# Optimization experiments

Hardware: AMD Instinct MI355X
Metric: run time of the kernel (lower is better)

## Reference

```python
import jax, jax.numpy as jnp
import numpy as np

N, INC, INN, OUTC, OUTN, MAXD = 8, 64, 20000, 64, 8000, 32


def setup_inputs() -> dict:
    key = jax.random.key(0)
    k0, k1, k2, k3, k4 = jax.random.split(key, 5)
    # adjacency list: outn nodes, degree in [8, 32], padded to MAXD with index 0
    rng = np.random.default_rng(0)
    deg = rng.integers(8, MAXD + 1, size=OUTN)                      # (outn,)
    A_np = rng.integers(0, INN, size=(OUTN, MAXD))                  # (outn, maxD)
    valid = np.arange(MAXD)[None, :] < deg[:, None]
    A_np = np.where(valid, A_np, 0)
    # '_norm' option: mask entries are 1/degree for valid slots, 0 for pad
    mask_np = valid.astype(np.float32) / deg[:, None].astype(np.float32)

    x = jax.random.normal(k0, (N, INC, INN), dtype=jnp.float32)
    # hadamard weight: sqrt(2/inn) * U(-1, 1)
    weight = np.sqrt(2.0 / INN).astype(np.float32) * (
        2.0 * jax.random.uniform(k1, (INC, INN), dtype=jnp.float32) - 1.0)
    # weight_norm Linear(inc, outc): v (outc, inc) direction, g (outc,) magnitude
    ct_v = jax.random.normal(k2, (OUTC, INC), dtype=jnp.float32) * (1.0 / np.sqrt(INC).astype(np.float32))
    ct_g = 0.5 + jax.random.uniform(k3, (OUTC,), dtype=jnp.float32)
    bias = 0.2 * jax.random.normal(k4, (1, OUTC, OUTN), dtype=jnp.float32)
    return {
        'x': x,
        'weight': weight,
        'ct_v': ct_v,
        'ct_g': ct_g,
        'bias': bias,
        'mask': jnp.asarray(mask_np),
        'A': jnp.asarray(A_np, dtype=jnp.int32),
    }


def reference(x, weight, ct_v, ct_g, bias, mask, A):
    # x: (N, inc, inn); weight: (inc, inn)
    xw = x * weight                                   # hadamard
    gathered = xw[:, :, A]                            # (N, inc, outn, maxD) adjacency gather
    pooled = jnp.einsum('bcod,od->bco', gathered, mask)  # degree-normalized masked sum
    # weight_norm: W = g * v / ||v||_row
    W = ct_g[:, None] * ct_v / jnp.linalg.norm(ct_v, axis=1, keepdims=True)  # (outc, inc)
    y = jnp.einsum('bco,kc->bko', pooled, W)          # (N, outc, outn)
    return y + bias
```

## Files before the change

kernel.cpp:

```cpp
#include <hip/hip_runtime.h>
#include <stdint.h>

#define NB   8
#define INC  64
#define INN  20000
#define OUTC 64
#define OUTN 8000
#define MAXD 32

typedef float f32x2 __attribute__((ext_vector_type(2)));

__global__ __launch_bounds__(256)
void xt_prep_kernel(const float* __restrict__ x, const float* __restrict__ w,
                    const int* __restrict__ A, const float* __restrict__ mask,
                    const float* __restrict__ ct_v, const float* __restrict__ ct_g,
                    unsigned char* __restrict__ xT8, uint4* __restrict__ AQ4,
                    float2* __restrict__ scale2, float* __restrict__ W_T) {
    int t = threadIdx.x;
    if (blockIdx.y == 8) {
        int flat = blockIdx.x;
        if (flat == 64) {
            int k = t;
            if (k < OUTC) {
                float s = 0.f;
                for (int c = 0; c < INC; ++c) { float v = ct_v[k * INC + c]; s += v * v; }
                float inv = ct_g[k] / sqrtf(s);
                for (int c = 0; c < INC; ++c) W_T[c * OUTC + k] = ct_v[k * INC + c] * inv;
            }
            return;
        }
        if (flat > 64 || t >= 128) return;
        int o = flat * 128 + t;
        if (o >= OUTN) return;
        const int4* arow = (const int4*)(A + (size_t)o * MAXD);
#pragma unroll
        for (int j = 0; j < 4; ++j) {
            int4 v0 = arow[2 * j];
            int4 v1 = arow[2 * j + 1];
            uint4 pk;
            pk.x = (uint32_t)v0.x | ((uint32_t)v0.y << 16);
            pk.y = (uint32_t)v0.z | ((uint32_t)v0.w << 16);
            pk.z = (uint32_t)v1.x | ((uint32_t)v1.y << 16);
            pk.w = (uint32_t)v1.z | ((uint32_t)v1.w << 16);
            AQ4[(size_t)o * 4 + j] = pk;
        }
        float invdeg = mask[(size_t)o * MAXD];
        float deg    = rintf(1.0f / invdeg);
        scale2[o] = make_float2(invdeg * (1.0f / 256.0f), 32.0f - deg);
        return;
    }

    __shared__ float tile[64][68];
    int b  = blockIdx.y;
    int i0 = blockIdx.x * 64;
    int il = (t & 15) * 4;
    int cb = t >> 4;

#pragma unroll
    for (int cl = 0; cl < 4; ++cl) {
        int c = cb + cl * 16;
        int i = i0 + il;
        if (i < INN) {
            float4 xv = *(const float4*)(x + ((size_t)b * INC + c) * INN + i);
            float4 wv = *(const float4*)(w + (size_t)c * INN + i);
            float4 p = make_float4(xv.x * wv.x * 256.0f, xv.y * wv.y * 256.0f,
                                   xv.z * wv.z * 256.0f, xv.w * wv.w * 256.0f);
            *(float4*)(&tile[c][il]) = p;
        }
    }
    __syncthreads();

    int i_loc = t >> 2;
    int h     = t & 3;
    int i     = i0 + i_loc;
    if (i < INN) {
        int c0 = h * 16;
        float s[16];
#pragma unroll
        for (int j = 0; j < 16; ++j) s[j] = tile[c0 + j][i_loc];
        uint4 out;
        uint32_t u;
        u = __builtin_amdgcn_cvt_pk_fp8_f32(s[0],  s[1],  0, false);
        u = __builtin_amdgcn_cvt_pk_fp8_f32(s[2],  s[3],  u, true);
        out.x = u;
        u = __builtin_amdgcn_cvt_pk_fp8_f32(s[4],  s[5],  0, false);
        u = __builtin_amdgcn_cvt_pk_fp8_f32(s[6],  s[7],  u, true);
        out.y = u;
        u = __builtin_amdgcn_cvt_pk_fp8_f32(s[8],  s[9],  0, false);
        u = __builtin_amdgcn_cvt_pk_fp8_f32(s[10], s[11], u, true);
        out.z = u;
        u = __builtin_amdgcn_cvt_pk_fp8_f32(s[12], s[13], 0, false);
        u = __builtin_amdgcn_cvt_pk_fp8_f32(s[14], s[15], u, true);
        out.w = u;
        *(uint4*)(xT8 + ((size_t)(b * INN + i)) * 64 + h * 16) = out;
    }
}

__global__ __launch_bounds__(256, 4)
void gather_kernel(const unsigned char* __restrict__ xT8, const uint4* __restrict__ AQ4,
                   const float2* __restrict__ scale2, float* __restrict__ pooled) {
    __shared__ float trans[32][68];
    int flat  = blockIdx.x;
    int b     = flat & 7;
    int chunk = flat >> 3;
    int o0    = chunk * 32;
    int t     = threadIdx.x;
    int lane  = t & 63;
    int wid   = t >> 6;
    int osub  = lane >> 3;
    int chgrp = lane & 7;
    int oloc  = wid * 8 + osub;
    int o     = o0 + oloc;

    const char* xTb = (const char*)xT8 + (size_t)b * INN * 64 + chgrp * 8;

    const uint4* aq = AQ4 + (size_t)o * 4;
    uint4 q0 = aq[0], q1 = aq[1], q2 = aq[2], q3 = aq[3];
    float2 sc = scale2[o];
    uint2  zw = *(const uint2*)(xTb);

    float a0 = 0.f, a1 = 0.f, a2 = 0.f, a3 = 0.f;
    float a4 = 0.f, a5 = 0.f, a6 = 0.f, a7 = 0.f;

#define DOI(idx)                                                        \
    {                                                                   \
        uint2 v = *(const uint2*)(xTb + ((size_t)(idx) << 6));          \
        f32x2 e;                                                        \
        e = __builtin_amdgcn_cvt_pk_f32_fp8(v.x, false);                \
        a0 += e.x; a1 += e.y;                                           \
        e = __builtin_amdgcn_cvt_pk_f32_fp8(v.x, true);                 \
        a2 += e.x; a3 += e.y;                                           \
        e = __builtin_amdgcn_cvt_pk_f32_fp8(v.y, false);                \
        a4 += e.x; a5 += e.y;                                           \
        e = __builtin_amdgcn_cvt_pk_f32_fp8(v.y, true);                 \
        a6 += e.x; a7 += e.y;                                           \
    }
#define DOU(u) DOI((u) & 0xFFFFu) DOI((u) >> 16)
    DOU(q0.x) DOU(q0.y) DOU(q0.z) DOU(q0.w)
    DOU(q1.x) DOU(q1.y) DOU(q1.z) DOU(q1.w)
    DOU(q2.x) DOU(q2.y) DOU(q2.z) DOU(q2.w)
    DOU(q3.x) DOU(q3.y) DOU(q3.z) DOU(q3.w)
#undef DOU
#undef DOI

    f32x2 e0 = __builtin_amdgcn_cvt_pk_f32_fp8(zw.x, false);
    f32x2 e1 = __builtin_amdgcn_cvt_pk_f32_fp8(zw.x, true);
    f32x2 e2 = __builtin_amdgcn_cvt_pk_f32_fp8(zw.y, false);
    f32x2 e3 = __builtin_amdgcn_cvt_pk_f32_fp8(zw.y, true);
    float4 r0 = make_float4((a0 - sc.y * e0.x) * sc.x, (a1 - sc.y * e0.y) * sc.x,
                            (a2 - sc.y * e1.x) * sc.x, (a3 - sc.y * e1.y) * sc.x);
    float4 r1 = make_float4((a4 - sc.y * e2.x) * sc.x, (a5 - sc.y * e2.y) * sc.x,
                            (a6 - sc.y * e3.x) * sc.x, (a7 - sc.y * e3.y) * sc.x);
    *(float4*)(&trans[oloc][chgrp * 8])     = r0;
    *(float4*)(&trans[oloc][chgrp * 8 + 4]) = r1;
    __syncthreads();

#pragma unroll
    for (int rep = 0; rep < 2; ++rep) {
        int j  = t + rep * 256;
        int c  = j >> 3;
        int oq = (j & 7) * 4;
        float4 v = make_float4(trans[oq][c], trans[oq + 1][c],
                               trans[oq + 2][c], trans[oq + 3][c]);
        *(float4*)(pooled + ((size_t)(b * OUTC + c)) * OUTN + o0 + oq) = v;
    }
}

__global__ __launch_bounds__(256)
void out_kernel(float* io, const float* __restrict__ W_T,
                const float* __restrict__ bias) {
    __shared__ __align__(16) float sp[INC][128];
    __shared__ __align__(16) float sw[INC][OUTC];
    int obase = blockIdx.x * 128;
    int b     = blockIdx.y;

    const float* pb = io + (size_t)b * INC * OUTN;
    for (int idx = threadIdx.x; idx < INC * 32; idx += 256) {
        int c  = idx >> 5;
        int q  = idx & 31;
        int o4 = obase + q * 4;
        float4 v = (o4 < OUTN) ? *(const float4*)(pb + (size_t)c * OUTN + o4)
                               : make_float4(0.f, 0.f, 0.f, 0.f);
        *(float4*)(&sp[c][q * 4]) = v;
    }
    for (int idx = threadIdx.x; idx < (INC * OUTC) / 4; idx += 256) {
        ((float4*)sw)[idx] = ((const float4*)W_T)[idx];
    }
    __syncthreads();

    int t   = threadIdx.x;
    int kt  = t >> 4;
    int ot0 = (t & 15) * 8;
    int k0  = kt * 4;

    float acc[4][8];
#pragma unroll
    for (int kk = 0; kk < 4; ++kk) {
#pragma unroll
        for (int jh = 0; jh < 2; ++jh) {
            int o4 = obase + ot0 + jh * 4;
            float4 bv = (o4 < OUTN)
                ? *(const float4*)(bias + (size_t)(k0 + kk) * OUTN + o4)
                : make_float4(0.f, 0.f, 0.f, 0.f);
            acc[kk][jh * 4 + 0] = bv.x;
            acc[kk][jh * 4 + 1] = bv.y;
            acc[kk][jh * 4 + 2] = bv.z;
            acc[kk][jh * 4 + 3] = bv.w;
        }
    }

#pragma unroll 4
    for (int c = 0; c < INC; ++c) {
        float4 w4  = *(const float4*)(&sw[c][k0]);
        float4 pa  = *(const float4*)(&sp[c][ot0]);
        float4 pb4 = *(const float4*)(&sp[c][ot0 + 4]);
        float p[8] = {pa.x, pa.y, pa.z, pa.w, pb4.x, pb4.y, pb4.z, pb4.w};
        float wv[4] = {w4.x, w4.y, w4.z, w4.w};
#pragma unroll
        for (int kk = 0; kk < 4; ++kk)
#pragma unroll
            for (int j = 0; j < 8; ++j)
                acc[kk][j] += wv[kk] * p[j];
    }

    int o0 = obase + ot0;
    if (o0 < OUTN) {
#pragma unroll
        for (int kk = 0; kk < 4; ++kk) {
            float4 s0 = make_float4(acc[kk][0], acc[kk][1], acc[kk][2], acc[kk][3]);
            float4 s1 = make_float4(acc[kk][4], acc[kk][5], acc[kk][6], acc[kk][7]);
            float* dst = io + ((size_t)(b * OUTC + k0 + kk)) * OUTN + o0;
            *(float4*)(dst)     = s0;
            *(float4*)(dst + 4) = s1;
        }
    }
}

extern "C" void kernel_launch(void* const* d_in, const int* in_sizes, int n_in,
                              void* d_out, int out_size, void* d_ws, size_t ws_size,
                              hipStream_t stream) {
    const float* x    = (const float*)d_in[0];
    const float* w    = (const float*)d_in[1];
    const float* ct_v = (const float*)d_in[2];
    const float* ct_g = (const float*)d_in[3];
    const float* bias = (const float*)d_in[4];
    const float* mask = (const float*)d_in[5];
    const int*   A    = (const int*)d_in[6];
    float* y = (float*)d_out;

    char* ws = (char*)d_ws;
    unsigned char* xT8 = (unsigned char*)(ws);
    uint4*  AQ4    = (uint4*)(ws + 10240000);
    float2* scale2 = (float2*)(ws + 10752000);
    float*  W_T    = (float*)(ws + 10816000);

    xt_prep_kernel<<<dim3(313, 9), 256, 0, stream>>>(x, w, A, mask, ct_v, ct_g,
                                                     xT8, AQ4, scale2, W_T);
    gather_kernel<<<2000, 256, 0, stream>>>(xT8, AQ4, scale2, y);
    out_kernel<<<dim3(63, NB), 256, 0, stream>>>(y, W_T, bias);
}
```

Measured before the change: 48.39 us.

## Interleave batches in fp8 transposed x so one gather row serves all batches

The fp8 transposed input is relaid out as node-major with all 8 batches contiguous (512 bytes per node). The gather kernel now handles 8 output nodes across all batches per block, with wave-uniform adjacency offsets (pre-shifted by 9) loaded via readfirstlane into scalar registers, and each lane reads 8 bytes of a 512-byte row. This makes each neighbor fetch one contiguous 512-byte access instead of 8 scattered 64-byte ones, and amortizes index loads across batches. The cost is larger index storage (32-bit instead of packed 16-bit), a different shared-memory transpose, and higher occupancy pressure from launch bounds 6.

Result: slower. 55.64 us (+15.0%).

```diff
diff --git a/kernel.cpp b/kernel.cpp
--- a/kernel.cpp
+++ b/kernel.cpp
@@ -34,15 +34,11 @@
         if (o >= OUTN) return;
         const int4* arow = (const int4*)(A + (size_t)o * MAXD);
 #pragma unroll
-        for (int j = 0; j < 4; ++j) {
-            int4 v0 = arow[2 * j];
-            int4 v1 = arow[2 * j + 1];
-            uint4 pk;
-            pk.x = (uint32_t)v0.x | ((uint32_t)v0.y << 16);
-            pk.y = (uint32_t)v0.z | ((uint32_t)v0.w << 16);
-            pk.z = (uint32_t)v1.x | ((uint32_t)v1.y << 16);
-            pk.w = (uint32_t)v1.z | ((uint32_t)v1.w << 16);
-            AQ4[(size_t)o * 4 + j] = pk;
+        for (int j = 0; j < 8; ++j) {
+            int4 v = arow[j];
+            uint4 pk = make_uint4((uint32_t)v.x << 9, (uint32_t)v.y << 9,
+                                  (uint32_t)v.z << 9, (uint32_t)v.w << 9);
+            AQ4[(size_t)o * 8 + j] = pk;
         }
         float invdeg = mask[(size_t)o * MAXD];
         float deg    = rintf(1.0f / invdeg);
@@ -92,77 +88,70 @@
         u = __builtin_amdgcn_cvt_pk_fp8_f32(s[12], s[13], 0, false);
         u = __builtin_amdgcn_cvt_pk_fp8_f32(s[14], s[15], u, true);
         out.w = u;
-        *(uint4*)(xT8 + ((size_t)(b * INN + i)) * 64 + h * 16) = out;
-    }
-}
-
-__global__ __launch_bounds__(256, 4)
-void gather_kernel(const unsigned char* __restrict__ xT8, const uint4* __restrict__ AQ4,
+        *(uint4*)(xT8 + (size_t)i * 512 + b * 64 + h * 16) = out;
+    }
+}
+
+__global__ __launch_bounds__(256, 6)
+void gather_kernel(const unsigned char* __restrict__ xT8, const uint32_t* __restrict__ AQ32,
                    const float2* __restrict__ scale2, float* __restrict__ pooled) {
-    __shared__ float trans[32][68];
-    int flat  = blockIdx.x;
-    int b     = flat & 7;
-    int chunk = flat >> 3;
-    int o0    = chunk * 32;
-    int t     = threadIdx.x;
-    int lane  = t & 63;
-    int wid   = t >> 6;
-    int osub  = lane >> 3;
-    int chgrp = lane & 7;
-    int oloc  = wid * 8 + osub;
-    int o     = o0 + oloc;
-
-    const char* xTb = (const char*)xT8 + (size_t)b * INN * 64 + chgrp * 8;
-
-    const uint4* aq = AQ4 + (size_t)o * 4;
-    uint4 q0 = aq[0], q1 = aq[1], q2 = aq[2], q3 = aq[3];
-    float2 sc = scale2[o];
-    uint2  zw = *(const uint2*)(xTb);
-
-    float a0 = 0.f, a1 = 0.f, a2 = 0.f, a3 = 0.f;
-    float a4 = 0.f, a5 = 0.f, a6 = 0.f, a7 = 0.f;
-
-#define DOI(idx)                                                        \
-    {                                                                   \
-        uint2 v = *(const uint2*)(xTb + ((size_t)(idx) << 6));          \
-        f32x2 e;                                                        \
-        e = __builtin_amdgcn_cvt_pk_f32_fp8(v.x, false);                \
-        a0 += e.x; a1 += e.y;                                           \
-        e = __builtin_amdgcn_cvt_pk_f32_fp8(v.x, true);                 \
-        a2 += e.x; a3 += e.y;                                           \
-        e = __builtin_amdgcn_cvt_pk_f32_fp8(v.y, false);                \
-        a4 += e.x; a5 += e.y;                                           \
-        e = __builtin_amdgcn_cvt_pk_f32_fp8(v.y, true);                 \
-        a6 += e.x; a7 += e.y;                                           \
-    }
-#define DOU(u) DOI((u) & 0xFFFFu) DOI((u) >> 16)
-    DOU(q0.x) DOU(q0.y) DOU(q0.z) DOU(q0.w)
-    DOU(q1.x) DOU(q1.y) DOU(q1.z) DOU(q1.w)
-    DOU(q2.x) DOU(q2.y) DOU(q2.z) DOU(q2.w)
-    DOU(q3.x) DOU(q3.y) DOU(q3.z) DOU(q3.w)
-#undef DOU
-#undef DOI
-
-    f32x2 e0 = __builtin_amdgcn_cvt_pk_f32_fp8(zw.x, false);
-    f32x2 e1 = __builtin_amdgcn_cvt_pk_f32_fp8(zw.x, true);
-    f32x2 e2 = __builtin_amdgcn_cvt_pk_f32_fp8(zw.y, false);
-    f32x2 e3 = __builtin_amdgcn_cvt_pk_f32_fp8(zw.y, true);
-    float4 r0 = make_float4((a0 - sc.y * e0.x) * sc.x, (a1 - sc.y * e0.y) * sc.x,
-                            (a2 - sc.y * e1.x) * sc.x, (a3 - sc.y * e1.y) * sc.x);
-    float4 r1 = make_float4((a4 - sc.y * e2.x) * sc.x, (a5 - sc.y * e2.y) * sc.x,
-                            (a6 - sc.y * e3.x) * sc.x, (a7 - sc.y * e3.y) * sc.x);
-    *(float4*)(&trans[oloc][chgrp * 8])     = r0;
-    *(float4*)(&trans[oloc][chgrp * 8 + 4]) = r1;
+    __shared__ float trans[8][516];
+    int t    = threadIdx.x;
+    int lane = t & 63;
+    int wid  = t >> 6;
+    int o0   = blockIdx.x * 8;
+    uint32_t laneoff = (uint32_t)lane * 8u;
+
+    uint2 zv = *(const uint2*)(xT8 + laneoff);
+    f32x2 z01 = __builtin_amdgcn_cvt_pk_f32_fp8(zv.x, false);
+    f32x2 z23 = __builtin_amdgcn_cvt_pk_f32_fp8(zv.x, true);
+    f32x2 z45 = __builtin_amdgcn_cvt_pk_f32_fp8(zv.y, false);
+    f32x2 z67 = __builtin_amdgcn_cvt_pk_f32_fp8(zv.y, true);
+
+#pragma unroll
+    for (int oi = 0; oi < 2; ++oi) {
+        int oloc = wid * 2 + oi;
+        int ou   = __builtin_amdgcn_readfirstlane(o0 + oloc);
+        const uint32_t* aq = AQ32 + (size_t)ou * 32;
+        float2 sc = scale2[ou];
+
+        f32x2 a01 = {0.f, 0.f}, a23 = {0.f, 0.f}, a45 = {0.f, 0.f}, a67 = {0.f, 0.f};
+#pragma unroll
+        for (int d = 0; d < 32; ++d) {
+            uint2 v = *(const uint2*)(xT8 + (aq[d] + laneoff));
+            a01 += __builtin_amdgcn_cvt_pk_f32_fp8(v.x, false);
+            a23 += __builtin_amdgcn_cvt_pk_f32_fp8(v.x, true);
+            a45 += __builtin_amdgcn_cvt_pk_f32_fp8(v.y, false);
+            a67 += __builtin_amdgcn_cvt_pk_f32_fp8(v.y, true);
+        }
+        float4 r0 = make_float4((a01.x - sc.y * z01.x) * sc.x,
+                                (a01.y - sc.y * z01.y) * sc.x,
+                                (a23.x - sc.y * z23.x) * sc.x,
+                                (a23.y - sc.y * z23.y) * sc.x);
+        float4 r1 = make_float4((a45.x - sc.y * z45.x) * sc.x,
+                                (a45.y - sc.y * z45.y) * sc.x,
+                                (a67.x - sc.y * z67.x) * sc.x,
+                                (a67.y - sc.y * z67.y) * sc.x);
+        float* row = trans[oloc];
+        *(float4*)(&row[lane * 4])       = r0;
+        *(float4*)(&row[256 + lane * 4]) = r1;
+    }
     __syncthreads();
 
 #pragma unroll
     for (int rep = 0; rep < 2; ++rep) {
-        int j  = t + rep * 256;
-        int c  = j >> 3;
-        int oq = (j & 7) * 4;
-        float4 v = make_float4(trans[oq][c], trans[oq + 1][c],
-                               trans[oq + 2][c], trans[oq + 3][c]);
-        *(float4*)(pooled + ((size_t)(b * OUTC + c)) * OUTN + o0 + oq) = v;
+        int p   = t + rep * 256;
+        int b   = p >> 6;
+        int c   = p & 63;
+        int oct = c >> 3;
+        int j   = c & 7;
+        int base = (j >= 4 ? 256 + (j - 4) : j) + (b * 8 + oct) * 4;
+        float v[8];
+#pragma unroll
+        for (int o = 0; o < 8; ++o) v[o] = trans[o][base];
+        float* dst = pooled + ((size_t)(b * OUTC + c)) * OUTN + o0;
+        *(float4*)(dst)     = make_float4(v[0], v[1], v[2], v[3]);
+        *(float4*)(dst + 4) = make_float4(v[4], v[5], v[6], v[7]);
     }
 }
 
@@ -250,12 +239,12 @@
 
     char* ws = (char*)d_ws;
     unsigned char* xT8 = (unsigned char*)(ws);
-    uint4*  AQ4    = (uint4*)(ws + 10240000);
-    float2* scale2 = (float2*)(ws + 10752000);
-    float*  W_T    = (float*)(ws + 10816000);
+    uint32_t* AQ32  = (uint32_t*)(ws + 10240000);
+    float2*   scale2 = (float2*)(ws + 11264000);
+    float*    W_T    = (float*)(ws + 11328000);
 
     xt_prep_kernel<<<dim3(313, 9), 256, 0, stream>>>(x, w, A, mask, ct_v, ct_g,
-                                                     xT8, AQ4, scale2, W_T);
-    gather_kernel<<<2000, 256, 0, stream>>>(xT8, AQ4, scale2, y);
+                                                     xT8, (uint4*)AQ32, scale2, W_T);
+    gather_kernel<<<1000, 256, 0, stream>>>(xT8, AQ32, scale2, y);
     out_kernel<<<dim3(63, NB), 256, 0, stream>>>(y, W_T, bias);
 }
```
